# Optimization experiments

Measured on AMD Instinct MI355X. Metric: run time of the kernel, lower is better.

Reference implementation:

```python
import jax, jax.numpy as jnp
import numpy as np

MAX_DET = 100
IOU_THR = 0.5


def _iou_matrix(b):
    # b: [N,4] xyxy -> [N,N] pairwise IoU
    area = jnp.clip(b[:, 2] - b[:, 0], 0) * jnp.clip(b[:, 3] - b[:, 1], 0)
    lt = jnp.maximum(b[:, None, :2], b[None, :, :2])
    rb = jnp.minimum(b[:, None, 2:], b[None, :, 2:])
    wh = jnp.clip(rb - lt, 0)
    inter = wh[..., 0] * wh[..., 1]
    union = area[:, None] + area[None, :] - inter
    return inter / jnp.maximum(union, 1e-8)


def _batched_nms(boxes, scores, classes, iou_thr, max_out):
    # torchvision batched_nms semantics: offset boxes by class id so
    # boxes of different classes never overlap, then greedy NMS.
    n = boxes.shape[0]
    order = jnp.argsort(-scores)
    b = boxes[order]
    c = classes[order]
    off = c.astype(b.dtype) * (jnp.max(b) + 1.0)
    iou = _iou_matrix(b + off[:, None])  # [N,N]

    def body(valid, _):
        idx = jnp.argmax(valid)          # highest-score surviving candidate
        any_valid = jnp.any(valid)
        new_valid = valid & ~(iou[idx] > iou_thr)
        new_valid = new_valid.at[idx].set(False)
        sel = jnp.where(any_valid, order[idx], -1)
        return new_valid, sel

    _, sel = jax.lax.scan(body, jnp.ones(n, dtype=bool), None, length=max_out)
    return sel  # [max_out] indices into original order, -1 padded


def _detect_one(cls_o, box_o, idx, cls_ids, scale, size, anchor_boxes):
    a = anchor_boxes[idx]  # [N,4] yxyx
    yc_a = (a[:, 0] + a[:, 2]) * 0.5
    xc_a = (a[:, 1] + a[:, 3]) * 0.5
    ha = a[:, 2] - a[:, 0]
    wa = a[:, 3] - a[:, 1]
    box = box_o.astype(jnp.float32)
    ty, tx, th, tw = box[:, 0], box[:, 1], box[:, 2], box[:, 3]
    w = jnp.exp(tw) * wa
    h = jnp.exp(th) * ha
    yc = ty * ha + yc_a
    xc = tx * wa + xc_a
    boxes = jnp.stack([xc - w * 0.5, yc - h * 0.5, xc + w * 0.5, yc + h * 0.5], axis=1)
    # clip_boxes_xyxy with size = img_size / img_scale
    sz = jnp.concatenate([size, size]) / scale  # [4]
    boxes = jnp.minimum(jnp.clip(boxes, 0), sz[None, :])
    scores = jax.nn.sigmoid(cls_o[:, 0]).astype(jnp.float32)
    sel = _batched_nms(boxes, scores, cls_ids, IOU_THR, MAX_DET)
    safe = jnp.maximum(sel, 0)
    valid = (sel >= 0).astype(jnp.float32)[:, None]
    det = jnp.concatenate([
        boxes[safe] * scale,
        scores[safe][:, None],
        (cls_ids[safe] + 1).astype(jnp.float32)[:, None],
    ], axis=1)
    return det * valid  # zero-pad rows past num_det


def setup_inputs() -> dict:
    key = jax.random.key(0)
    ks = jax.random.split(key, 7)
    B, N, A, C = 8, 4096, 49104, 90
    cls_outputs = jax.random.normal(ks[0], (B, N, 1), jnp.float32)
    box_outputs = jax.random.normal(ks[1], (B, N, 4), jnp.float32) * 0.2
    indices = jax.random.randint(ks[2], (B, N), 0, A)
    classes = jax.random.randint(ks[3], (B, N), 0, C)
    # anchor boxes in yxyx, roughly covering a 512x512 image
    ctr = jax.random.uniform(ks[4], (A, 2), jnp.float32, 0.0, 512.0)
    hw = jax.random.uniform(ks[5], (A, 2), jnp.float32, 16.0, 128.0)
    anchor_boxes = jnp.concatenate([ctr - hw * 0.5, ctr + hw * 0.5], axis=1)
    img_scale = jax.random.uniform(ks[6], (B,), jnp.float32, 0.5, 1.5)
    img_size = jnp.full((B, 2), 512.0, jnp.float32)
    return dict(cls_outputs=cls_outputs, box_outputs=box_outputs,
                indices=indices, classes=classes, anchor_boxes=anchor_boxes,
                img_scale=img_scale, img_size=img_size)


def reference(cls_outputs, box_outputs, indices, classes, anchor_boxes, img_scale, img_size):
    f = jax.vmap(_detect_one, in_axes=(0, 0, 0, 0, 0, 0, None))
    return f(cls_outputs, box_outputs, indices, classes, img_scale, img_size, anchor_boxes)
```

## Files before the change

kernel.cpp:

```cpp
#include <hip/hip_runtime.h>
#include <stdint.h>

#define N_DET    4096
#define HALF     2048
#define MAX_DET  100
#define NTHREADS 1024
#define SORT_THREADS 512
#define DEC_THREADS 256
#define DEC_CHUNKS  16
#define IOU_THR  0.5f

typedef unsigned long long u64;

__device__ __forceinline__ float fadd(float a, float b) { return __fadd_rn(a, b); }
__device__ __forceinline__ float fsub(float a, float b) { return __fsub_rn(a, b); }
__device__ __forceinline__ float fmul(float a, float b) { return __fmul_rn(a, b); }

struct Box { float x1, y1, x2, y2; };

__device__ __forceinline__ Box decode_box(const float* __restrict__ box_b,
                                          const int*   __restrict__ idx_b,
                                          const float* __restrict__ anchors,
                                          int i, float sz0, float sz1)
{
    int ai = idx_b[i];
    float a0 = anchors[ai * 4 + 0];
    float a1 = anchors[ai * 4 + 1];
    float a2 = anchors[ai * 4 + 2];
    float a3 = anchors[ai * 4 + 3];
    float yc_a = fmul(fadd(a0, a2), 0.5f);
    float xc_a = fmul(fadd(a1, a3), 0.5f);
    float ha = fsub(a2, a0);
    float wa = fsub(a3, a1);
    float ty = box_b[i * 4 + 0];
    float tx = box_b[i * 4 + 1];
    float th = box_b[i * 4 + 2];
    float tw = box_b[i * 4 + 3];
    float we = fmul(expf(tw), wa);
    float he = fmul(expf(th), ha);
    float yc = fadd(fmul(ty, ha), yc_a);
    float xc = fadd(fmul(tx, wa), xc_a);
    Box r;
    r.x1 = fsub(xc, fmul(we, 0.5f));
    r.y1 = fsub(yc, fmul(he, 0.5f));
    r.x2 = fadd(xc, fmul(we, 0.5f));
    r.y2 = fadd(yc, fmul(he, 0.5f));
    r.x1 = fminf(fmaxf(r.x1, 0.f), sz0);
    r.y1 = fminf(fmaxf(r.y1, 0.f), sz1);
    r.x2 = fminf(fmaxf(r.x2, 0.f), sz0);
    r.y2 = fminf(fmaxf(r.y2, 0.f), sz1);
    return r;
}

__device__ __forceinline__ float sigmoidf_ref(float x)
{
    return __fdiv_rn(1.0f, __fadd_rn(1.0f, expf(-x)));
}

__device__ __forceinline__ bool iou_suppress(float hx1, float hy1, float hx2, float hy2, float har,
                                             float cx1, float cy1, float cx2, float cy2, float car)
{
    float lt0 = fmaxf(hx1, cx1);
    float lt1 = fmaxf(hy1, cy1);
    float rb0 = fminf(hx2, cx2);
    float rb1 = fminf(hy2, cy2);
    float w0 = fmaxf(fsub(rb0, lt0), 0.f);
    float w1 = fmaxf(fsub(rb1, lt1), 0.f);
    float inter = fmul(w0, w1);
    float uni = fsub(fadd(har, car), inter);
    float iou = __fdiv_rn(inter, fmaxf(uni, 1e-8f));
    return iou > IOU_THR;
}

__device__ __forceinline__ u64 shfl_xor_u64(u64 x, int mask)
{
    unsigned lo = (unsigned)x, hi = (unsigned)(x >> 32);
    lo = __shfl_xor(lo, mask, 64);
    hi = __shfl_xor(hi, mask, 64);
    return ((u64)hi << 32) | lo;
}

__device__ __forceinline__ void cex(u64& a, u64& b, bool desc)
{
    bool sw = desc ? (a < b) : (a > b);
    u64 ta = a, tb = b;
    a = sw ? tb : ta;
    b = sw ? ta : tb;
}

__device__ __forceinline__ void shuf_pass(u64 e[4], int d, bool desc, int l)
{
    bool lower = ((l & d) == 0);
    bool keepmax = (desc == lower);
    #pragma unroll
    for (int s = 0; s < 4; ++s) {
        u64 p = shfl_xor_u64(e[s], d);
        u64 mx = (e[s] > p) ? e[s] : p;
        u64 mn = (e[s] < p) ? e[s] : p;
        e[s] = keepmax ? mx : mn;
    }
}

__device__ __forceinline__ void shuf_pass2(u64 e[2], int d, int l)
{
    bool keepmax = ((l & d) == 0);
    #pragma unroll
    for (int s = 0; s < 2; ++s) {
        u64 p = shfl_xor_u64(e[s], d);
        u64 mx = (e[s] > p) ? e[s] : p;
        u64 mn = (e[s] < p) ? e[s] : p;
        e[s] = keepmax ? mx : mn;
    }
}

__global__ __launch_bounds__(DEC_THREADS)
void decode_kernel(const float* __restrict__ cls_outputs,
                   const float* __restrict__ box_outputs,
                   const int*   __restrict__ indices,
                   const float* __restrict__ anchors,
                   const float* __restrict__ img_scale,
                   const float* __restrict__ img_size,
                   float*       __restrict__ wmax,
                   u64*         __restrict__ wkeys,
                   float4*      __restrict__ wboxes)
{
    const int blk   = blockIdx.x;
    const int b     = blk / DEC_CHUNKS;
    const int chunk = blk % DEC_CHUNKS;
    const int i     = chunk * DEC_THREADS + threadIdx.x;

    const float* cls_b = cls_outputs + (size_t)b * N_DET;
    const float* box_b = box_outputs + (size_t)b * N_DET * 4;
    const int*   idx_b = indices + (size_t)b * N_DET;
    const float  scale = img_scale[b];
    const float  sz0   = __fdiv_rn(img_size[b * 2 + 0], scale);
    const float  sz1   = __fdiv_rn(img_size[b * 2 + 1], scale);

    Box r = decode_box(box_b, idx_b, anchors, i, sz0, sz1);
    float sc = sigmoidf_ref(cls_b[i]);

    wboxes[(size_t)b * N_DET + i] = make_float4(r.x1, r.y1, r.x2, r.y2);
    wkeys[(size_t)b * N_DET + i] =
        ((u64)__float_as_uint(sc) << 32) | (unsigned)(N_DET - 1 - i);

    float lmax = fmaxf(fmaxf(r.x1, r.y1), fmaxf(r.x2, r.y2));
    for (int o = 32; o; o >>= 1) lmax = fmaxf(lmax, __shfl_xor(lmax, o, 64));
    __shared__ float wred[DEC_THREADS / 64];
    if ((threadIdx.x & 63) == 0) wred[threadIdx.x >> 6] = lmax;
    __syncthreads();
    if (threadIdx.x == 0) {
        float m = wred[0];
        #pragma unroll
        for (int k = 1; k < DEC_THREADS / 64; ++k) m = fmaxf(m, wred[k]);
        wmax[b * DEC_CHUNKS + chunk] = m;
    }
}

__global__ __launch_bounds__(SORT_THREADS, 1)
void sort_half_kernel(u64* __restrict__ wkeys)
{
    __shared__ u64 keys[HALF];
    u64* gk = wkeys + (size_t)blockIdx.x * HALF;
    const int t = threadIdx.x;
    const int l = t & 63;

    u64 e[4];
    #pragma unroll
    for (int s = 0; s < 4; ++s) e[s] = gk[4 * t + s];

    cex(e[0], e[1], true);
    cex(e[2], e[3], false);
    for (int k = 4; k <= 128; k <<= 1) {
        bool desc = (l & (k >> 2)) == 0;
        for (int j = k >> 1; j >= 4; j >>= 1) shuf_pass(e, j >> 2, desc, l);
        cex(e[0], e[2], desc); cex(e[1], e[3], desc);
        cex(e[0], e[1], desc); cex(e[2], e[3], desc);
    }
    {
        bool desc = ((t >> 6) & 1) == 0;
        for (int j = 128; j >= 4; j >>= 1) shuf_pass(e, j >> 2, desc, l);
        cex(e[0], e[2], desc); cex(e[1], e[3], desc);
        cex(e[0], e[1], desc); cex(e[2], e[3], desc);
    }
    #pragma unroll
    for (int s = 0; s < 4; ++s) keys[4 * t + s] = e[s];

    for (int k = 512; k <= HALF; k <<= 1) {
        for (int j = k >> 1; j >= 256; j >>= 1) {
            __syncthreads();
            #pragma unroll
            for (int vv = 0; vv < 2; ++vv) {
                int v = t + vv * SORT_THREADS;
                int i   = ((v & ~(j - 1)) << 1) | (v & (j - 1));
                int ixj = i | j;
                bool desc = ((i & k) == 0);
                u64 a = keys[i], c = keys[ixj];
                bool sw = desc ? (a < c) : (a > c);
                if (sw) { keys[i] = c; keys[ixj] = a; }
            }
        }
        __syncthreads();
        u64 f[4];
        #pragma unroll
        for (int s = 0; s < 4; ++s) f[s] = keys[4 * t + s];
        bool desc = (t & (k >> 2)) == 0;
        for (int j = 128; j >= 4; j >>= 1) shuf_pass(f, j >> 2, desc, l);
        cex(f[0], f[2], desc); cex(f[1], f[3], desc);
        cex(f[0], f[1], desc); cex(f[2], f[3], desc);
        #pragma unroll
        for (int s = 0; s < 4; ++s) keys[4 * t + s] = f[s];
    }
    __syncthreads();
    #pragma unroll
    for (int s = 0; s < 4; ++s) gk[4 * t + s] = keys[4 * t + s];
}

__global__ __launch_bounds__(NTHREADS, 1)
void scan_kernel(const int*    __restrict__ classes,
                 const float*  __restrict__ img_scale,
                 const float*  __restrict__ wmax,
                 const u64*    __restrict__ wkeys,
                 const float4* __restrict__ wboxes,
                 float*        __restrict__ out)
{
    __shared__ u64    mstream[1024];
    __shared__ int    waveA[8];
    __shared__ float4 bbox[64];
    __shared__ float  barr[64];
    __shared__ int    borig[64];
    __shared__ u64    bkey[64];
    __shared__ u64    extp[16];
    __shared__ unsigned Cplo[16][64];
    __shared__ unsigned Cphi[16][64];
    __shared__ int    sel[MAX_DET];
    __shared__ float  selsc[MAX_DET];
    __shared__ float4 hbox4[MAX_DET];
    __shared__ float  harr[MAX_DET];
    __shared__ int    sh_count;

    const int b = blockIdx.x;
    const int t = threadIdx.x;
    const int l = t & 63;

    const int*    cls_id_b = classes + (size_t)b * N_DET;
    const float   scale    = img_scale[b];
    const u64*    gA = wkeys + (size_t)b * N_DET;
    const u64*    gB = gA + HALF;
    const float4* wb = wboxes + (size_t)b * N_DET;

    float mm = wmax[b * DEC_CHUNKS + 0];
    #pragma unroll
    for (int k = 1; k < DEC_CHUNKS; ++k) mm = fmaxf(mm, wmax[b * DEC_CHUNKS + k]);
    const float M = fadd(mm, 1.0f);

    if (t < 512) mstream[t] = gA[t];
    else         mstream[t] = gB[511 - (t - 512)];
    if (t < MAX_DET) sel[t] = -1;
    if (t == 0) sh_count = 0;
    __syncthreads();

    {
        if (t < 512) {
            u64 a = mstream[t], c = mstream[t + 512];
            if (a < c) { mstream[t] = c; mstream[t + 512] = a; }
        }
        __syncthreads();
        if (t < 512) {
            int i   = ((t & ~255) << 1) | (t & 255);
            int ixj = i | 256;
            u64 a = mstream[i], c = mstream[ixj];
            if (a < c) { mstream[i] = c; mstream[ixj] = a; }
        }
        __syncthreads();
        if (t < 256) {
            u64 f[4];
            #pragma unroll
            for (int s = 0; s < 4; ++s) f[s] = mstream[4 * t + s];
            for (int j = 128; j >= 4; j >>= 1) shuf_pass(f, j >> 2, true, l);
            cex(f[0], f[2], true); cex(f[1], f[3], true);
            cex(f[0], f[1], true); cex(f[2], f[3], true);
            #pragma unroll
            for (int s = 0; s < 4; ++s) mstream[4 * t + s] = f[s];
        }
        __syncthreads();
    }

    {
        bool isA = false;
        if (t < 512) {
            int orig = N_DET - 1 - (int)(unsigned)(mstream[t] & 0xFFFFFFFFull);
            isA = (orig < HALF);
        }
        u64 bal = __ballot(isA ? 1 : 0);
        if ((t & 63) == 0 && (t >> 6) < 8) waveA[t >> 6] = __popcll(bal);
        __syncthreads();
    }
    int pa = 0;
    #pragma unroll
    for (int w = 0; w < 8; ++w) pa += waveA[w];
    int pb = 512 - pa;

    const int j = t & 63;
    const int g = t >> 6;

    for (int c = 0; c < N_DET; c += 64) {
        int count = sh_count;
        if (count >= MAX_DET) break;

        if (c + 64 <= 512) {
            if (t < 64) {
                u64 key = mstream[c + t];
                int orig = N_DET - 1 - (int)(unsigned)(key & 0xFFFFFFFFull);
                bkey[t] = key; borig[t] = orig;
                float4 bb = wb[orig];
                float off = fmul((float)cls_id_b[orig], M);
                float x1 = fadd(bb.x, off), y1 = fadd(bb.y, off);
                float x2 = fadd(bb.z, off), y2 = fadd(bb.w, off);
                bbox[t] = make_float4(x1, y1, x2, y2);
                barr[t] = fmul(fmaxf(fsub(x2, x1), 0.f), fmaxf(fsub(y2, y1), 0.f));
            }
        } else {
            if (t < 64) {
                u64 ee[2];
                if (l < 32) {
                    int p0 = pa + 2 * l;
                    ee[0] = (p0     < HALF) ? gA[p0]     : 0ull;
                    ee[1] = (p0 + 1 < HALF) ? gA[p0 + 1] : 0ull;
                } else {
                    int p  = 2 * (l - 32);
                    int q0 = pb + 63 - p;
                    ee[0] = (q0     < HALF) ? gB[q0]     : 0ull;
                    ee[1] = (q0 - 1 < HALF && q0 - 1 >= 0) ? gB[q0 - 1] : 0ull;
                }
                shuf_pass2(ee, 32, l); shuf_pass2(ee, 16, l); shuf_pass2(ee, 8, l);
                shuf_pass2(ee, 4, l);  shuf_pass2(ee, 2, l);  shuf_pass2(ee, 1, l);
                cex(ee[0], ee[1], true);

                int orig0 = N_DET - 1 - (int)(unsigned)(ee[0] & 0xFFFFFFFFull);
                int orig1 = N_DET - 1 - (int)(unsigned)(ee[1] & 0xFFFFFFFFull);
                bool r0 = (l < 32) && (ee[0] != 0ull);
                bool r1 = (l < 32) && (ee[1] != 0ull);
                if (l < 32) {
                    #pragma unroll
                    for (int s = 0; s < 2; ++s) {
                        int  r    = 2 * l + s;
                        u64  key  = s ? ee[1] : ee[0];
                        int  orig = s ? orig1 : orig0;
                        bool ok   = s ? r1 : r0;
                        bkey[r] = key;
                        if (ok) {
                            float4 bb = wb[orig];
                            float off = fmul((float)cls_id_b[orig], M);
                            float x1 = fadd(bb.x, off), y1 = fadd(bb.y, off);
                            float x2 = fadd(bb.z, off), y2 = fadd(bb.w, off);
                            bbox[r] = make_float4(x1, y1, x2, y2);
                            barr[r] = fmul(fmaxf(fsub(x2, x1), 0.f), fmaxf(fsub(y2, y1), 0.f));
                            borig[r] = orig;
                        } else {
                            bbox[r] = make_float4(0.f, 0.f, 0.f, 0.f);
                            barr[r] = 0.f;
                            borig[r] = -1;
                        }
                    }
                }
                u64 bR0 = __ballot(r0), bR1 = __ballot(r1);
                u64 bA0 = __ballot(r0 && (orig0 < HALF));
                u64 bA1 = __ballot(r1 && (orig1 < HALF));
                int real = __popcll(bR0) + __popcll(bR1);
                int aw   = __popcll(bA0) + __popcll(bA1);
                pa += aw;
                pb += real - aw;
            }
        }
        __syncthreads();

        float4 c4  = bbox[j];
        float  car = barr[j];
        const bool valid = (borig[j] >= 0);

        bool sup = !valid;
        for (int k = g; k < count; k += 16) {
            float4 h4 = hbox4[k];
            sup = sup | iou_suppress(h4.x, h4.y, h4.z, h4.w, harr[k],
                                     c4.x, c4.y, c4.z, c4.w, car);
        }
        u64 bal = __ballot(sup ? 1 : 0);
        if ((t & 63) == 0) extp[g] = bal;

        unsigned cplo = 0, cphi = 0;
        for (int r = g + 1; r < 64; r += 16) {
            int q = j ^ r;
            float4 q4 = bbox[q];
            float qar = barr[q];
            bool hit = (q > j) & valid & (borig[q] >= 0) &
                       iou_suppress(c4.x, c4.y, c4.z, c4.w, car,
                                    q4.x, q4.y, q4.z, q4.w, qar);
            unsigned bit = hit ? 1u : 0u;
            if (q < 32) cplo |= bit << q; else cphi |= bit << (q - 32);
        }
        Cplo[g][j] = cplo;
        Cphi[g][j] = cphi;
        __syncthreads();

        if (t < 64) {
            const int lane = t;
            u64 ext = 0;
            #pragma unroll
            for (int gg = 0; gg < 16; ++gg) ext |= extp[gg];
            unsigned lo = 0, hi = 0;
            #pragma unroll
            for (int gg = 0; gg < 16; ++gg) { lo |= Cplo[gg][lane]; hi |= Cphi[gg][lane]; }
            u64 C = ((u64)hi << 32) | lo;
            u64 hasC = __ballot(C != 0ull);

            u64 alive = ~ext;
            u64 selmask = 0;
            int total = count;
            while (alive && total < MAX_DET) {
                int k = __ffsll(alive) - 1;
                selmask |= (1ull << k);
                alive &= ~(1ull << k);
                ++total;
                if ((hasC >> k) & 1ull) {
                    unsigned clo = __shfl((int)(unsigned)C, k, 64);
                    unsigned chi = __shfl((int)(unsigned)(C >> 32), k, 64);
                    alive &= ~(((u64)chi << 32) | clo);
                }
            }

            if ((selmask >> lane) & 1ull) {
                int p = count + __popcll(selmask & ((1ull << lane) - 1ull));
                hbox4[p] = bbox[lane];
                harr[p]  = barr[lane];
                sel[p]   = borig[lane];
                selsc[p] = __uint_as_float((unsigned)(bkey[lane] >> 32));
            }
            if (lane == 0) sh_count = total;
        }
        __syncthreads();
    }

    if (t >= 64) return;
    for (int r = t; r < MAX_DET; r += 64) {
        int sidx = sel[r];
        float* o = out + (size_t)b * MAX_DET * 6 + (size_t)r * 6;
        if (sidx < 0) {
            o[0] = 0.f; o[1] = 0.f; o[2] = 0.f; o[3] = 0.f; o[4] = 0.f; o[5] = 0.f;
        } else {
            float4 bb = wb[sidx];
            int c = cls_id_b[sidx];
            o[0] = fmul(bb.x, scale);
            o[1] = fmul(bb.y, scale);
            o[2] = fmul(bb.z, scale);
            o[3] = fmul(bb.w, scale);
            o[4] = selsc[r];
            o[5] = (float)(c + 1);
        }
    }
}

extern "C" void kernel_launch(void* const* d_in, const int* in_sizes, int n_in,
                              void* d_out, int out_size, void* d_ws, size_t ws_size,
                              hipStream_t stream)
{
    const float* cls_outputs = (const float*)d_in[0];
    const float* box_outputs = (const float*)d_in[1];
    const int*   indices     = (const int*)d_in[2];
    const int*   classes     = (const int*)d_in[3];
    const float* anchors     = (const float*)d_in[4];
    const float* img_scale   = (const float*)d_in[5];
    const float* img_size    = (const float*)d_in[6];
    float*       out         = (float*)d_out;

    const int B = in_sizes[5];

    char* wsb = (char*)d_ws;
    float*  wmax   = (float*)wsb;
    u64*    wkeys  = (u64*)(wsb + 1024);
    float4* wboxes = (float4*)(wsb + 1024 + (size_t)B * N_DET * sizeof(u64));

    decode_kernel<<<dim3(B * DEC_CHUNKS), dim3(DEC_THREADS), 0, stream>>>(
        cls_outputs, box_outputs, indices, anchors, img_scale, img_size,
        wmax, wkeys, wboxes);

    sort_half_kernel<<<dim3(B * 2), dim3(SORT_THREADS), 0, stream>>>(wkeys);

    scan_kernel<<<dim3(B), dim3(NTHREADS), 0, stream>>>(
        classes, img_scale, wmax, wkeys, wboxes, out);
}
```

Before: 40.12 us.

## Fuse half-sort kernel into scan kernel using shared-memory keys

Removes the separate sort_half_kernel launch and performs both 2048-element bitonic sorts inside the scan kernel, with 1024 threads split into two 512-thread halves. The sorted keys stay in a 32 KB shared array, and later merge-stream reads come from shared memory instead of global memory. This drops one kernel launch and a global round trip of the keys. In exchange, the sort now runs on only B blocks instead of 2B, and the scan kernel uses more LDS.

```diff
diff --git a/kernel.cpp b/kernel.cpp
--- a/kernel.cpp
+++ b/kernel.cpp
@@ -5,7 +5,6 @@
 #define HALF     2048
 #define MAX_DET  100
 #define NTHREADS 1024
-#define SORT_THREADS 512
 #define DEC_THREADS 256
 #define DEC_CHUNKS  16
 #define IOU_THR  0.5f
@@ -156,65 +155,6 @@
     }
 }
 
-__global__ __launch_bounds__(SORT_THREADS, 1)
-void sort_half_kernel(u64* __restrict__ wkeys)
-{
-    __shared__ u64 keys[HALF];
-    u64* gk = wkeys + (size_t)blockIdx.x * HALF;
-    const int t = threadIdx.x;
-    const int l = t & 63;
-
-    u64 e[4];
-    #pragma unroll
-    for (int s = 0; s < 4; ++s) e[s] = gk[4 * t + s];
-
-    cex(e[0], e[1], true);
-    cex(e[2], e[3], false);
-    for (int k = 4; k <= 128; k <<= 1) {
-        bool desc = (l & (k >> 2)) == 0;
-        for (int j = k >> 1; j >= 4; j >>= 1) shuf_pass(e, j >> 2, desc, l);
-        cex(e[0], e[2], desc); cex(e[1], e[3], desc);
-        cex(e[0], e[1], desc); cex(e[2], e[3], desc);
-    }
-    {
-        bool desc = ((t >> 6) & 1) == 0;
-        for (int j = 128; j >= 4; j >>= 1) shuf_pass(e, j >> 2, desc, l);
-        cex(e[0], e[2], desc); cex(e[1], e[3], desc);
-        cex(e[0], e[1], desc); cex(e[2], e[3], desc);
-    }
-    #pragma unroll
-    for (int s = 0; s < 4; ++s) keys[4 * t + s] = e[s];
-
-    for (int k = 512; k <= HALF; k <<= 1) {
-        for (int j = k >> 1; j >= 256; j >>= 1) {
-            __syncthreads();
-            #pragma unroll
-            for (int vv = 0; vv < 2; ++vv) {
-                int v = t + vv * SORT_THREADS;
-                int i   = ((v & ~(j - 1)) << 1) | (v & (j - 1));
-                int ixj = i | j;
-                bool desc = ((i & k) == 0);
-                u64 a = keys[i], c = keys[ixj];
-                bool sw = desc ? (a < c) : (a > c);
-                if (sw) { keys[i] = c; keys[ixj] = a; }
-            }
-        }
-        __syncthreads();
-        u64 f[4];
-        #pragma unroll
-        for (int s = 0; s < 4; ++s) f[s] = keys[4 * t + s];
-        bool desc = (t & (k >> 2)) == 0;
-        for (int j = 128; j >= 4; j >>= 1) shuf_pass(f, j >> 2, desc, l);
-        cex(f[0], f[2], desc); cex(f[1], f[3], desc);
-        cex(f[0], f[1], desc); cex(f[2], f[3], desc);
-        #pragma unroll
-        for (int s = 0; s < 4; ++s) keys[4 * t + s] = f[s];
-    }
-    __syncthreads();
-    #pragma unroll
-    for (int s = 0; s < 4; ++s) gk[4 * t + s] = keys[4 * t + s];
-}
-
 __global__ __launch_bounds__(NTHREADS, 1)
 void scan_kernel(const int*    __restrict__ classes,
                  const float*  __restrict__ img_scale,
@@ -223,6 +163,7 @@
                  const float4* __restrict__ wboxes,
                  float*        __restrict__ out)
 {
+    __shared__ u64    keys[N_DET];
     __shared__ u64    mstream[1024];
     __shared__ int    waveA[8];
     __shared__ float4 bbox[64];
@@ -238,14 +179,15 @@
     __shared__ float  harr[MAX_DET];
     __shared__ int    sh_count;
 
-    const int b = blockIdx.x;
-    const int t = threadIdx.x;
-    const int l = t & 63;
+    const int b  = blockIdx.x;
+    const int t  = threadIdx.x;
+    const int l  = t & 63;
+    const int th = t & 511;
+    const int hoff = (t >> 9) * HALF;
 
     const int*    cls_id_b = classes + (size_t)b * N_DET;
     const float   scale    = img_scale[b];
-    const u64*    gA = wkeys + (size_t)b * N_DET;
-    const u64*    gB = gA + HALF;
+    const u64*    wk = wkeys + (size_t)b * N_DET;
     const float4* wb = wboxes + (size_t)b * N_DET;
 
     float mm = wmax[b * DEC_CHUNKS + 0];
@@ -253,12 +195,59 @@
     for (int k = 1; k < DEC_CHUNKS; ++k) mm = fmaxf(mm, wmax[b * DEC_CHUNKS + k]);
     const float M = fadd(mm, 1.0f);
 
-    if (t < 512) mstream[t] = gA[t];
-    else         mstream[t] = gB[511 - (t - 512)];
+    u64 e[4];
+    #pragma unroll
+    for (int s = 0; s < 4; ++s) e[s] = wk[4 * t + s];
+
+    cex(e[0], e[1], true);
+    cex(e[2], e[3], false);
+    for (int k = 4; k <= 128; k <<= 1) {
+        bool desc = (l & (k >> 2)) == 0;
+        for (int j = k >> 1; j >= 4; j >>= 1) shuf_pass(e, j >> 2, desc, l);
+        cex(e[0], e[2], desc); cex(e[1], e[3], desc);
+        cex(e[0], e[1], desc); cex(e[2], e[3], desc);
+    }
+    {
+        bool desc = ((th >> 6) & 1) == 0;
+        for (int j = 128; j >= 4; j >>= 1) shuf_pass(e, j >> 2, desc, l);
+        cex(e[0], e[2], desc); cex(e[1], e[3], desc);
+        cex(e[0], e[1], desc); cex(e[2], e[3], desc);
+    }
+    #pragma unroll
+    for (int s = 0; s < 4; ++s) keys[4 * t + s] = e[s];
+
+    for (int k = 512; k <= HALF; k <<= 1) {
+        for (int j = k >> 1; j >= 256; j >>= 1) {
+            __syncthreads();
+            #pragma unroll
+            for (int vv = 0; vv < 2; ++vv) {
+                int v = th + vv * 512;
+                int i   = ((v & ~(j - 1)) << 1) | (v & (j - 1));
+                int ixj = i | j;
+                bool desc = ((i & k) == 0);
+                u64 a = keys[hoff + i], c = keys[hoff + ixj];
+                bool sw = desc ? (a < c) : (a > c);
+                if (sw) { keys[hoff + i] = c; keys[hoff + ixj] = a; }
+            }
+        }
+        __syncthreads();
+        u64 f[4];
+        #pragma unroll
+        for (int s = 0; s < 4; ++s) f[s] = keys[4 * t + s];
+        bool desc = (th & (k >> 2)) == 0;
+        for (int j = 128; j >= 4; j >>= 1) shuf_pass(f, j >> 2, desc, l);
+        cex(f[0], f[2], desc); cex(f[1], f[3], desc);
+        cex(f[0], f[1], desc); cex(f[2], f[3], desc);
+        #pragma unroll
+        for (int s = 0; s < 4; ++s) keys[4 * t + s] = f[s];
+    }
     if (t < MAX_DET) sel[t] = -1;
     if (t == 0) sh_count = 0;
     __syncthreads();
 
+    if (t < 512) mstream[t] = keys[t];
+    else         mstream[t] = keys[HALF + 511 - (t - 512)];
+    __syncthreads();
     {
         if (t < 512) {
             u64 a = mstream[t], c = mstream[t + 512];
@@ -324,13 +313,13 @@
                 u64 ee[2];
                 if (l < 32) {
                     int p0 = pa + 2 * l;
-                    ee[0] = (p0     < HALF) ? gA[p0]     : 0ull;
-                    ee[1] = (p0 + 1 < HALF) ? gA[p0 + 1] : 0ull;
+                    ee[0] = (p0     < HALF) ? keys[p0]     : 0ull;
+                    ee[1] = (p0 + 1 < HALF) ? keys[p0 + 1] : 0ull;
                 } else {
                     int p  = 2 * (l - 32);
                     int q0 = pb + 63 - p;
-                    ee[0] = (q0     < HALF) ? gB[q0]     : 0ull;
-                    ee[1] = (q0 - 1 < HALF && q0 - 1 >= 0) ? gB[q0 - 1] : 0ull;
+                    ee[0] = (q0     < HALF) ? keys[HALF + q0]     : 0ull;
+                    ee[1] = (q0 - 1 < HALF && q0 - 1 >= 0) ? keys[HALF + q0 - 1] : 0ull;
                 }
                 shuf_pass2(ee, 32, l); shuf_pass2(ee, 16, l); shuf_pass2(ee, 8, l);
                 shuf_pass2(ee, 4, l);  shuf_pass2(ee, 2, l);  shuf_pass2(ee, 1, l);
@@ -483,8 +472,6 @@
         cls_outputs, box_outputs, indices, anchors, img_scale, img_size,
         wmax, wkeys, wboxes);
 
-    sort_half_kernel<<<dim3(B * 2), dim3(SORT_THREADS), 0, stream>>>(wkeys);
-
     scan_kernel<<<dim3(B), dim3(NTHREADS), 0, stream>>>(
         classes, img_scale, wmax, wkeys, wboxes, out);
 }
```

Result: slower. 46.05 us (+14.8%).

## Fuse box decode into per-half bitonic sort kernel with vectorized loads

Applied to the files above, without the earlier changes.

Merges the decode kernel and the half-sort kernel into one launch: each 512-thread block decodes four detections per thread using vectorized float4/int4 loads, builds sort keys in registers and sorts them directly, skipping the global round-trip of unsorted keys. The per-chunk max reduction is folded into the same block, so the scan kernel now reads two partial maxima instead of sixteen. This removes a kernel launch and a key write/read. The trade-off is that decode now runs on only 16 blocks instead of 128, lowering parallelism for the gather-heavy decode phase.

```diff
diff --git a/kernel.cpp b/kernel.cpp
--- a/kernel.cpp
+++ b/kernel.cpp
@@ -6,8 +6,6 @@
 #define MAX_DET  100
 #define NTHREADS 1024
 #define SORT_THREADS 512
-#define DEC_THREADS 256
-#define DEC_CHUNKS  16
 #define IOU_THR  0.5f
 
 typedef unsigned long long u64;
@@ -18,24 +16,14 @@
 
 struct Box { float x1, y1, x2, y2; };
 
-__device__ __forceinline__ Box decode_box(const float* __restrict__ box_b,
-                                          const int*   __restrict__ idx_b,
-                                          const float* __restrict__ anchors,
-                                          int i, float sz0, float sz1)
-{
-    int ai = idx_b[i];
-    float a0 = anchors[ai * 4 + 0];
-    float a1 = anchors[ai * 4 + 1];
-    float a2 = anchors[ai * 4 + 2];
-    float a3 = anchors[ai * 4 + 3];
-    float yc_a = fmul(fadd(a0, a2), 0.5f);
-    float xc_a = fmul(fadd(a1, a3), 0.5f);
-    float ha = fsub(a2, a0);
-    float wa = fsub(a3, a1);
-    float ty = box_b[i * 4 + 0];
-    float tx = box_b[i * 4 + 1];
-    float th = box_b[i * 4 + 2];
-    float tw = box_b[i * 4 + 3];
+__device__ __forceinline__ Box decode_box_v(const float4 bo, const float4 a,
+                                            float sz0, float sz1)
+{
+    float yc_a = fmul(fadd(a.x, a.z), 0.5f);
+    float xc_a = fmul(fadd(a.y, a.w), 0.5f);
+    float ha = fsub(a.z, a.x);
+    float wa = fsub(a.w, a.y);
+    float ty = bo.x, tx = bo.y, th = bo.z, tw = bo.w;
     float we = fmul(expf(tw), wa);
     float he = fmul(expf(th), ha);
     float yc = fadd(fmul(ty, ha), yc_a);
@@ -113,21 +101,25 @@
     }
 }
 
-__global__ __launch_bounds__(DEC_THREADS)
-void decode_kernel(const float* __restrict__ cls_outputs,
-                   const float* __restrict__ box_outputs,
-                   const int*   __restrict__ indices,
-                   const float* __restrict__ anchors,
-                   const float* __restrict__ img_scale,
-                   const float* __restrict__ img_size,
-                   float*       __restrict__ wmax,
-                   u64*         __restrict__ wkeys,
-                   float4*      __restrict__ wboxes)
-{
-    const int blk   = blockIdx.x;
-    const int b     = blk / DEC_CHUNKS;
-    const int chunk = blk % DEC_CHUNKS;
-    const int i     = chunk * DEC_THREADS + threadIdx.x;
+__global__ __launch_bounds__(SORT_THREADS, 1)
+void dec_sort_kernel(const float* __restrict__ cls_outputs,
+                     const float* __restrict__ box_outputs,
+                     const int*   __restrict__ indices,
+                     const float* __restrict__ anchors,
+                     const float* __restrict__ img_scale,
+                     const float* __restrict__ img_size,
+                     float*       __restrict__ wmax,
+                     u64*         __restrict__ wkeys,
+                     float4*      __restrict__ wboxes)
+{
+    __shared__ u64   keys[HALF];
+    __shared__ float wred[8];
+
+    const int blk  = blockIdx.x;
+    const int b    = blk >> 1;
+    const int base = (blk & 1) * HALF;
+    const int t    = threadIdx.x;
+    const int l    = t & 63;
 
     const float* cls_b = cls_outputs + (size_t)b * N_DET;
     const float* box_b = box_outputs + (size_t)b * N_DET * 4;
@@ -136,37 +128,25 @@
     const float  sz0   = __fdiv_rn(img_size[b * 2 + 0], scale);
     const float  sz1   = __fdiv_rn(img_size[b * 2 + 1], scale);
 
-    Box r = decode_box(box_b, idx_b, anchors, i, sz0, sz1);
-    float sc = sigmoidf_ref(cls_b[i]);
-
-    wboxes[(size_t)b * N_DET + i] = make_float4(r.x1, r.y1, r.x2, r.y2);
-    wkeys[(size_t)b * N_DET + i] =
-        ((u64)__float_as_uint(sc) << 32) | (unsigned)(N_DET - 1 - i);
-
-    float lmax = fmaxf(fmaxf(r.x1, r.y1), fmaxf(r.x2, r.y2));
+    u64 e[4];
+    float lmax = 0.0f;
+    const int4   idx4 = ((const int4*)(idx_b + base))[t];
+    const float4 cl4  = ((const float4*)(cls_b + base))[t];
+    const int   idxs[4] = { idx4.x, idx4.y, idx4.z, idx4.w };
+    const float cls4[4] = { cl4.x, cl4.y, cl4.z, cl4.w };
+    #pragma unroll
+    for (int s = 0; s < 4; ++s) {
+        int i = base + 4 * t + s;
+        float4 bo = ((const float4*)box_b)[i];
+        float4 an = ((const float4*)anchors)[idxs[s]];
+        Box r = decode_box_v(bo, an, sz0, sz1);
+        wboxes[(size_t)b * N_DET + i] = make_float4(r.x1, r.y1, r.x2, r.y2);
+        lmax = fmaxf(lmax, fmaxf(fmaxf(r.x1, r.y1), fmaxf(r.x2, r.y2)));
+        float sc = sigmoidf_ref(cls4[s]);
+        e[s] = ((u64)__float_as_uint(sc) << 32) | (unsigned)(N_DET - 1 - i);
+    }
     for (int o = 32; o; o >>= 1) lmax = fmaxf(lmax, __shfl_xor(lmax, o, 64));
-    __shared__ float wred[DEC_THREADS / 64];
-    if ((threadIdx.x & 63) == 0) wred[threadIdx.x >> 6] = lmax;
-    __syncthreads();
-    if (threadIdx.x == 0) {
-        float m = wred[0];
-        #pragma unroll
-        for (int k = 1; k < DEC_THREADS / 64; ++k) m = fmaxf(m, wred[k]);
-        wmax[b * DEC_CHUNKS + chunk] = m;
-    }
-}
-
-__global__ __launch_bounds__(SORT_THREADS, 1)
-void sort_half_kernel(u64* __restrict__ wkeys)
-{
-    __shared__ u64 keys[HALF];
-    u64* gk = wkeys + (size_t)blockIdx.x * HALF;
-    const int t = threadIdx.x;
-    const int l = t & 63;
-
-    u64 e[4];
-    #pragma unroll
-    for (int s = 0; s < 4; ++s) e[s] = gk[4 * t + s];
+    if (l == 0) wred[t >> 6] = lmax;
 
     cex(e[0], e[1], true);
     cex(e[2], e[3], false);
@@ -211,8 +191,16 @@
         for (int s = 0; s < 4; ++s) keys[4 * t + s] = f[s];
     }
     __syncthreads();
+    u64* gk = wkeys + (size_t)b * N_DET + base;
     #pragma unroll
     for (int s = 0; s < 4; ++s) gk[4 * t + s] = keys[4 * t + s];
+
+    if (t == 0) {
+        float m = wred[0];
+        #pragma unroll
+        for (int k = 1; k < 8; ++k) m = fmaxf(m, wred[k]);
+        wmax[blk] = m;
+    }
 }
 
 __global__ __launch_bounds__(NTHREADS, 1)
@@ -248,10 +236,7 @@
     const u64*    gB = gA + HALF;
     const float4* wb = wboxes + (size_t)b * N_DET;
 
-    float mm = wmax[b * DEC_CHUNKS + 0];
-    #pragma unroll
-    for (int k = 1; k < DEC_CHUNKS; ++k) mm = fmaxf(mm, wmax[b * DEC_CHUNKS + k]);
-    const float M = fadd(mm, 1.0f);
+    const float M = fadd(fmaxf(wmax[b * 2 + 0], wmax[b * 2 + 1]), 1.0f);
 
     if (t < 512) mstream[t] = gA[t];
     else         mstream[t] = gB[511 - (t - 512)];
@@ -479,12 +464,10 @@
     u64*    wkeys  = (u64*)(wsb + 1024);
     float4* wboxes = (float4*)(wsb + 1024 + (size_t)B * N_DET * sizeof(u64));
 
-    decode_kernel<<<dim3(B * DEC_CHUNKS), dim3(DEC_THREADS), 0, stream>>>(
+    dec_sort_kernel<<<dim3(B * 2), dim3(SORT_THREADS), 0, stream>>>(
         cls_outputs, box_outputs, indices, anchors, img_scale, img_size,
         wmax, wkeys, wboxes);
 
-    sort_half_kernel<<<dim3(B * 2), dim3(SORT_THREADS), 0, stream>>>(wkeys);
-
     scan_kernel<<<dim3(B), dim3(NTHREADS), 0, stream>>>(
         classes, img_scale, wmax, wkeys, wboxes, out);
 }
```

Measured after the change: 37.47 us. 1.07x faster.
